# Performance work log

Hardware: AMD Instinct MI355X
Metric: run time of the kernel (lower is better)

The kernel has to match this reference:

```python
import jax, jax.numpy as jnp
import numpy as np

B, S, D = 4, 2048, 2048   # batch, seq, hidden
E, F, K = 8, 1024, 2      # experts, expert ffn dim, top-k
SF = 1024                 # shared-expert ffn dim
EPS = 1e-6


def setup_inputs() -> dict:
    key = jax.random.key(0)
    ks = jax.random.split(key, 9)
    g = lambda k, shape, scale: (jax.random.normal(k, shape, jnp.float32) * scale)
    return {
        "x": g(ks[0], (B, S, D), 1.0),
        "rms_weight": jnp.ones((D,), jnp.float32),
        "router_w": g(ks[1], (D, E), 0.02),
        "w_gate": g(ks[2], (E, D, F), 0.02),
        "w_up": g(ks[3], (E, D, F), 0.02),
        "w_down": g(ks[4], (E, F, D), 0.02),
        "sw_gate": g(ks[5], (D, SF), 0.02),
        "sw_up": g(ks[6], (D, SF), 0.02),
        "sw_down": g(ks[7], (SF, D), 0.02),
    }


def _rmsnorm(x, w, eps=EPS):
    var = jnp.mean(x * x, axis=-1, keepdims=True)
    return x * jax.lax.rsqrt(var + eps) * w


def reference(x, rms_weight, router_w, w_gate, w_up, w_down, sw_gate, sw_up, sw_down):
    b, s, d = x.shape
    e = router_w.shape[1]
    h = _rmsnorm(x, rms_weight)
    ht = h.reshape(-1, d)                      # [T, D] tokens
    t = ht.shape[0]

    # Router: softmax over experts, top-k, renormalize selected weights
    logits = ht @ router_w                     # [T, E]
    probs = jax.nn.softmax(logits, axis=-1)
    topv, topi = jax.lax.top_k(probs, K)       # [T, K]
    topv = topv / jnp.sum(topv, axis=-1, keepdims=True)
    # dense [T, E] combine weights (zero for non-selected experts)
    w_dense = jnp.zeros((t, e), ht.dtype).at[jnp.arange(t)[:, None], topi].set(topv)

    # Expert SwiGLU MLPs (grouped GEMM expressed densely over experts)
    g = jnp.einsum('td,edf->tef', ht, w_gate)  # [T, E, F]
    u = jnp.einsum('td,edf->tef', ht, w_up)
    eo = jnp.einsum('tef,efd->ted', jax.nn.silu(g) * u, w_down)  # [T, E, D]
    moe = jnp.einsum('te,ted->td', w_dense, eo)                   # weighted combine

    # Shared expert (SwiGLU)
    sh = (jax.nn.silu(ht @ sw_gate) * (ht @ sw_up)) @ sw_down

    return (moe + sh).reshape(b, s, d)
```

## Files before the change

kernel.cpp:

```cpp
#include <hip/hip_runtime.h>
#include <stdint.h>

#define T_TOK 8192
#define DDIM  2048
#define NEXP  8
#define FDIM  1024
#define CAP   25600
#define NT_M  200
#define BK    64
#define GXT   16
#define NBLK  (GXT * NT_M)
#define CPX   (NBLK / 8)

typedef __bf16 bf16x8 __attribute__((ext_vector_type(8)));
typedef float  f32x4  __attribute__((ext_vector_type(4)));

typedef const __attribute__((address_space(1))) uint32_t* as1_u32;
typedef __attribute__((address_space(3))) uint32_t* as3_u32;

__device__ __forceinline__ void gload16(const void* g, void* l) {
  __builtin_amdgcn_global_load_lds((as1_u32)g, (as3_u32)l, 16, 0, 0);
}
__device__ __forceinline__ float bf2f(uint16_t u) {
  union { uint32_t i; float f; } v; v.i = ((uint32_t)u) << 16; return v.f;
}
__device__ __forceinline__ uint16_t f2bf(float f) {
  union { float f; uint32_t i; } v; v.f = f;
  uint32_t i = v.i;
  i += 0x7FFFu + ((i >> 16) & 1u);
  return (uint16_t)(i >> 16);
}

__global__ __launch_bounds__(256) void k_rms_router(
    const float* __restrict__ x, const float* __restrict__ rmsw,
    const float* __restrict__ router_w, uint16_t* __restrict__ h,
    int* __restrict__ topi, float* __restrict__ topw, int* __restrict__ counts)
{
  int wv = threadIdx.x >> 6, lane = threadIdx.x & 63;
  int t = blockIdx.x * 4 + wv;
  const float* xr = x + (size_t)t * DDIM;

  float4 xv[8], wv8[8];
  #pragma unroll
  for (int j = 0; j < 8; j++) {
    xv[j]  = ((const float4*)xr)[j * 64 + lane];
    wv8[j] = ((const float4*)rmsw)[j * 64 + lane];
  }
  float ss = 0.f;
  #pragma unroll
  for (int j = 0; j < 8; j++)
    ss += xv[j].x * xv[j].x + xv[j].y * xv[j].y + xv[j].z * xv[j].z + xv[j].w * xv[j].w;
  #pragma unroll
  for (int m = 32; m >= 1; m >>= 1) ss += __shfl_xor(ss, m, 64);
  float scale = rsqrtf(ss * (1.0f / DDIM) + 1e-6f);

  float hv[8][4];
  #pragma unroll
  for (int j = 0; j < 8; j++) {
    hv[j][0] = xv[j].x * scale * wv8[j].x;
    hv[j][1] = xv[j].y * scale * wv8[j].y;
    hv[j][2] = xv[j].z * scale * wv8[j].z;
    hv[j][3] = xv[j].w * scale * wv8[j].w;
    ushort4 hw;
    hw.x = f2bf(hv[j][0]); hw.y = f2bf(hv[j][1]);
    hw.z = f2bf(hv[j][2]); hw.w = f2bf(hv[j][3]);
    ((ushort4*)(h + (size_t)t * DDIM))[j * 64 + lane] = hw;
  }

  float lp[8] = {0, 0, 0, 0, 0, 0, 0, 0};
  #pragma unroll
  for (int j = 0; j < 8; j++) {
    #pragma unroll
    for (int c = 0; c < 4; c++) {
      int d = (j * 64 + lane) * 4 + c;
      const float* rw = router_w + (size_t)d * NEXP;
      float4 a = ((const float4*)rw)[0];
      float4 b = ((const float4*)rw)[1];
      float hj = hv[j][c];
      lp[0] += hj * a.x; lp[1] += hj * a.y; lp[2] += hj * a.z; lp[3] += hj * a.w;
      lp[4] += hj * b.x; lp[5] += hj * b.y; lp[6] += hj * b.z; lp[7] += hj * b.w;
    }
  }
  #pragma unroll
  for (int m = 32; m >= 1; m >>= 1) {
    #pragma unroll
    for (int e = 0; e < 8; e++) lp[e] += __shfl_xor(lp[e], m, 64);
  }
  if (lane == 0) {
    int i0 = 0;
    for (int e = 1; e < 8; e++) if (lp[e] > lp[i0]) i0 = e;
    int i1 = (i0 == 0) ? 1 : 0;
    for (int e = 0; e < 8; e++) if (e != i0 && lp[e] > lp[i1]) i1 = e;
    float p0 = 1.f / (1.f + expf(lp[i1] - lp[i0]));
    topi[t * 2] = i0; topi[t * 2 + 1] = i1;
    topw[t * 2] = p0; topw[t * 2 + 1] = 1.f - p0;
    atomicAdd(&counts[i0], 1);
    atomicAdd(&counts[i1], 1);
  }
}

__global__ void k_offsets(const int* __restrict__ counts, int* __restrict__ off) {
  if (threadIdx.x == 0 && blockIdx.x == 0) {
    int o = 0;
    for (int e = 0; e < NEXP; e++) { off[e] = o; o += (counts[e] + 127) & ~127; }
    off[8] = o;
    off[9] = o + T_TOK;
  }
}

__global__ __launch_bounds__(256) void k_scatter(
    const int* __restrict__ topi, const float* __restrict__ topw,
    const int* __restrict__ off, int* __restrict__ cursor,
    int* __restrict__ tokslot, float* __restrict__ wtrow)
{
  int idx = blockIdx.x * 256 + threadIdx.x;
  if (idx < T_TOK * 2) {
    int t = idx >> 1, k = idx & 1;
    int e = topi[idx];
    int slot = atomicAdd(&cursor[e], 1);
    int row = off[e] + slot;
    tokslot[row] = t * 4 + k;
    wtrow[row] = topw[idx];
  } else {
    int t = idx - T_TOK * 2;
    int row = off[8] + t;
    tokslot[row] = t * 4 + 2;
    wtrow[row] = 1.0f;
  }
}

__global__ __launch_bounds__(256) void k_tr_df(
    const float* __restrict__ wg, const float* __restrict__ wu,
    const float* __restrict__ sg, const float* __restrict__ su,
    uint16_t* __restrict__ wgT, uint16_t* __restrict__ wuT,
    uint16_t* __restrict__ sgT, uint16_t* __restrict__ suT)
{
  __shared__ float tile[32][33];
  int z = blockIdx.z;
  const float* src; uint16_t* dst;
  if (z < 8)       { src = wg + (size_t)z * DDIM * FDIM;       dst = wgT + (size_t)z * FDIM * DDIM; }
  else if (z < 16) { src = wu + (size_t)(z - 8) * DDIM * FDIM; dst = wuT + (size_t)(z - 8) * FDIM * DDIM; }
  else if (z == 16){ src = sg; dst = sgT; }
  else             { src = su; dst = suT; }
  int c0 = blockIdx.x * 32, r0 = blockIdx.y * 32;
  int tx = threadIdx.x & 31, ty = threadIdx.x >> 5;
  #pragma unroll
  for (int i = 0; i < 4; i++)
    tile[ty + 8 * i][tx] = src[(size_t)(r0 + ty + 8 * i) * FDIM + c0 + tx];
  __syncthreads();
  #pragma unroll
  for (int i = 0; i < 4; i++)
    dst[(size_t)(c0 + ty + 8 * i) * DDIM + r0 + tx] = f2bf(tile[tx][ty + 8 * i]);
}

__global__ __launch_bounds__(256) void k_tr_fd(
    const float* __restrict__ wd, const float* __restrict__ sd,
    uint16_t* __restrict__ wdT, uint16_t* __restrict__ sdT)
{
  __shared__ float tile[32][33];
  int z = blockIdx.z;
  const float* src; uint16_t* dst;
  if (z < 8) { src = wd + (size_t)z * FDIM * DDIM; dst = wdT + (size_t)z * DDIM * FDIM; }
  else       { src = sd; dst = sdT; }
  int c0 = blockIdx.x * 32, r0 = blockIdx.y * 32;
  int tx = threadIdx.x & 31, ty = threadIdx.x >> 5;
  #pragma unroll
  for (int i = 0; i < 4; i++)
    tile[ty + 8 * i][tx] = src[(size_t)(r0 + ty + 8 * i) * DDIM + c0 + tx];
  __syncthreads();
  #pragma unroll
  for (int i = 0; i < 4; i++)
    dst[(size_t)(c0 + ty + 8 * i) * FDIM + r0 + tx] = f2bf(tile[tx][ty + 8 * i]);
}

#define BUFA(c) (ldsu + (size_t)(c) * 16384)
#define BUFB(c) (ldsu + 8192 + (size_t)(c) * 16384)

#define XCD_REMAP()                                                            \
  int flat_ = blockIdx.y * GXT + blockIdx.x;                                   \
  int nf_ = (flat_ & 7) * CPX + (flat_ >> 3);                                  \
  int bx = nf_ & (GXT - 1);                                                    \
  int by = nf_ / GXT;

#define STAGE8(T, C) do {                                                     \
  _Pragma("unroll") for (int i_ = 0; i_ < 4; i_++) {                          \
    int G_ = w * 256 + i_ * 64 + lane;                                        \
    gload16(aSrc[i_] + (size_t)(T) * BK, BUFA(C) + G_ * 8);                   \
    gload16(bSrc[i_] + (size_t)(T) * BK, BUFB(C) + G_ * 8);                   \
  } } while (0)

#define COMPUTE_TILE(curA, curB) do {                                         \
  _Pragma("unroll") for (int ks_ = 0; ks_ < 2; ks_++) {                       \
    int ce_ = ks_ * 32 + ((lane >> 4) << 3);                                  \
    bf16x8 av_[4], bv_[4];                                                    \
    _Pragma("unroll") for (int m_ = 0; m_ < 4; m_++) {                        \
      int rr_ = wr * 64 + m_ * 16 + (lane & 15);                              \
      av_[m_] = *(const bf16x8*)((curA) + rr_ * 64 + (ce_ ^ ((rr_ & 7) << 3))); \
    }                                                                         \
    _Pragma("unroll") for (int n_ = 0; n_ < 4; n_++) {                        \
      int rr_ = wc * 64 + n_ * 16 + (lane & 15);                              \
      bv_[n_] = *(const bf16x8*)((curB) + rr_ * 64 + (ce_ ^ ((rr_ & 7) << 3))); \
    }                                                                         \
    __builtin_amdgcn_s_setprio(1);                                            \
    _Pragma("unroll") for (int m_ = 0; m_ < 4; m_++)                          \
    _Pragma("unroll") for (int n_ = 0; n_ < 4; n_++)                          \
      acc[m_][n_] = __builtin_amdgcn_mfma_f32_16x16x32_bf16(av_[m_], bv_[n_], acc[m_][n_], 0, 0, 0); \
    __builtin_amdgcn_s_setprio(0);                                            \
  } } while (0)

__global__ __launch_bounds__(256, 2) void k_stage1(
    const uint16_t* __restrict__ h, const uint16_t* __restrict__ wgT,
    const uint16_t* __restrict__ wuT, const uint16_t* __restrict__ sgT,
    const uint16_t* __restrict__ suT, const int* __restrict__ off,
    const int* __restrict__ tokslot, uint16_t* __restrict__ A_int)
{
  __shared__ __align__(16) uint16_t ldsu[32768];

  XCD_REMAP();
  int row0 = by * 128;
  int end = off[9];
  if (row0 >= end) return;
  int e = 0;
  #pragma unroll 1
  for (; e < 9; e++) if (row0 >= off[e] && row0 < off[e + 1]) break;
  const uint16_t* bg = (e < NEXP) ? wgT + (size_t)e * FDIM * DDIM : sgT;
  const uint16_t* bu = (e < NEXP) ? wuT + (size_t)e * FDIM * DDIM : suT;
  int f0 = bx * 64;

  int tid = threadIdx.x, lane = tid & 63, w = tid >> 6;
  int wr = w & 1, wc = w >> 1;

  const uint16_t* aSrc[4];
  const uint16_t* bSrc[4];
  #pragma unroll
  for (int i = 0; i < 4; i++) {
    int G = w * 256 + i * 64 + lane;
    int r = G >> 3, sl = G & 7;
    int gl = sl ^ (r & 7);
    int ts = tokslot[row0 + r];
    int tok = ts < 0 ? 0 : (ts >> 2);
    aSrc[i] = h + (size_t)tok * DDIM + gl * 8;
    int b = r >> 4;
    int fc = f0 + ((b >> 1) << 4) + (r & 15);
    const uint16_t* wbase = (b & 1) ? bu : bg;
    bSrc[i] = wbase + (size_t)fc * DDIM + gl * 8;
  }

  f32x4 acc[4][4] = {};
  const int NT = DDIM / BK;

  STAGE8(0, 0);
  __syncthreads();

  #pragma unroll 1
  for (int t = 0; t < NT; ++t) {
    int cur = t & 1;
    if (t + 1 < NT) STAGE8(t + 1, cur ^ 1);
    const uint16_t* curA = BUFA(cur);
    const uint16_t* curB = BUFB(cur);
    COMPUTE_TILE(curA, curB);
    __syncthreads();
  }

  #pragma unroll
  for (int m = 0; m < 4; m++) {
    #pragma unroll
    for (int p = 0; p < 2; p++) {
      #pragma unroll
      for (int r = 0; r < 4; r++) {
        int row = row0 + wr * 64 + m * 16 + ((lane >> 4) << 2) + r;
        int col = f0 + wc * 32 + p * 16 + (lane & 15);
        float g = acc[m][2 * p][r];
        float u = acc[m][2 * p + 1][r];
        float a = (g / (1.f + expf(-g))) * u;
        A_int[(size_t)row * FDIM + col] = f2bf(a);
      }
    }
  }
}

__global__ __launch_bounds__(256, 2) void k_stage2(
    const uint16_t* __restrict__ A_int, const uint16_t* __restrict__ wdT,
    const uint16_t* __restrict__ sdT, const int* __restrict__ off,
    const int* __restrict__ tokslot, const float* __restrict__ wtrow,
    uint16_t* __restrict__ eo, float* __restrict__ out)
{
  __shared__ __align__(16) uint16_t ldsu[32768];

  XCD_REMAP();
  int row0 = by * 128;
  int end = off[9];
  if (row0 >= end) return;
  int e = 0;
  #pragma unroll 1
  for (; e < 9; e++) if (row0 >= off[e] && row0 < off[e + 1]) break;
  const uint16_t* bw = (e < NEXP) ? wdT + (size_t)e * DDIM * FDIM : sdT;
  int d0 = bx * 128;

  int tid = threadIdx.x, lane = tid & 63, w = tid >> 6;
  int wr = w & 1, wc = w >> 1;

  const uint16_t* aSrc[4];
  const uint16_t* bSrc[4];
  #pragma unroll
  for (int i = 0; i < 4; i++) {
    int G = w * 256 + i * 64 + lane;
    int r = G >> 3, sl = G & 7;
    int gl = sl ^ (r & 7);
    aSrc[i] = A_int + (size_t)(row0 + r) * FDIM + gl * 8;
    bSrc[i] = bw + (size_t)(d0 + r) * FDIM + gl * 8;
  }

  f32x4 acc[4][4] = {};
  const int NT = FDIM / BK;

  STAGE8(0, 0);
  __syncthreads();

  #pragma unroll 1
  for (int t = 0; t < NT; ++t) {
    int cur = t & 1;
    if (t + 1 < NT) STAGE8(t + 1, cur ^ 1);
    const uint16_t* curA = BUFA(cur);
    const uint16_t* curB = BUFB(cur);
    COMPUTE_TILE(curA, curB);
    __syncthreads();
  }

  #pragma unroll
  for (int m = 0; m < 4; m++) {
    #pragma unroll
    for (int r = 0; r < 4; r++) {
      int grow = row0 + wr * 64 + m * 16 + ((lane >> 4) << 2) + r;
      int ts = tokslot[grow];
      if (ts < 0) continue;
      int tok = ts >> 2, slot = ts & 3;
      if (slot == 2) {
        size_t obase = (size_t)tok * DDIM;
        #pragma unroll
        for (int n = 0; n < 4; n++) {
          int col = d0 + wc * 64 + n * 16 + (lane & 15);
          out[obase + col] = acc[m][n][r];
        }
      } else {
        float wt = wtrow[grow];
        size_t obase = ((size_t)tok * 2 + slot) * DDIM;
        #pragma unroll
        for (int n = 0; n < 4; n++) {
          int col = d0 + wc * 64 + n * 16 + (lane & 15);
          eo[obase + col] = f2bf(acc[m][n][r] * wt);
        }
      }
    }
  }
}

__global__ __launch_bounds__(256) void k_final(
    const uint16_t* __restrict__ eo, float* __restrict__ out)
{
  int tok = blockIdx.x;
  int col = threadIdx.x * 8;
  const uint16_t* e0 = eo + ((size_t)tok * 2) * DDIM + col;
  const uint16_t* e1 = eo + ((size_t)tok * 2 + 1) * DDIM + col;
  float* op = out + (size_t)tok * DDIM + col;
  ushort4 a0 = *(const ushort4*)(e0);
  ushort4 a1 = *(const ushort4*)(e0 + 4);
  ushort4 b0 = *(const ushort4*)(e1);
  ushort4 b1 = *(const ushort4*)(e1 + 4);
  float4 s0 = *(const float4*)(op);
  float4 s1 = *(const float4*)(op + 4);
  float4 o0, o1;
  o0.x = s0.x + bf2f(a0.x) + bf2f(b0.x);
  o0.y = s0.y + bf2f(a0.y) + bf2f(b0.y);
  o0.z = s0.z + bf2f(a0.z) + bf2f(b0.z);
  o0.w = s0.w + bf2f(a0.w) + bf2f(b0.w);
  o1.x = s1.x + bf2f(a1.x) + bf2f(b1.x);
  o1.y = s1.y + bf2f(a1.y) + bf2f(b1.y);
  o1.z = s1.z + bf2f(a1.z) + bf2f(b1.z);
  o1.w = s1.w + bf2f(a1.w) + bf2f(b1.w);
  *(float4*)(op) = o0;
  *(float4*)(op + 4) = o1;
}

extern "C" void kernel_launch(void* const* d_in, const int* in_sizes, int n_in,
                              void* d_out, int out_size, void* d_ws, size_t ws_size,
                              hipStream_t stream) {
  (void)in_sizes; (void)n_in; (void)out_size;
  const float* x    = (const float*)d_in[0];
  const float* rmsw = (const float*)d_in[1];
  const float* rtw  = (const float*)d_in[2];
  const float* wg   = (const float*)d_in[3];
  const float* wu   = (const float*)d_in[4];
  const float* wd   = (const float*)d_in[5];
  const float* sg   = (const float*)d_in[6];
  const float* su   = (const float*)d_in[7];
  const float* sd   = (const float*)d_in[8];
  float* out = (float*)d_out;

  char* base = (char*)d_ws;
  size_t off_b = 0;
  auto place = [&](size_t bytes) { size_t r = off_b; off_b += (bytes + 255) & ~(size_t)255; return r; };
  size_t o_topi    = place((size_t)T_TOK * 2 * 4);
  size_t o_topw    = place((size_t)T_TOK * 2 * 4);
  size_t o_counts  = place(64);
  size_t o_offs    = place(64);
  size_t o_cursor  = place(64);
  size_t o_tokslot = place((size_t)CAP * 4);
  size_t o_wtrow   = place((size_t)CAP * 4);
  size_t o_h   = place((size_t)T_TOK * DDIM * 2);
  size_t o_wgT = place((size_t)NEXP * FDIM * DDIM * 2);
  size_t o_wuT = place((size_t)NEXP * FDIM * DDIM * 2);
  size_t o_sgT = place((size_t)FDIM * DDIM * 2);
  size_t o_suT = place((size_t)FDIM * DDIM * 2);
  size_t o_wdT = place((size_t)NEXP * DDIM * FDIM * 2);
  size_t o_sdT = place((size_t)DDIM * FDIM * 2);
  size_t o_Ai  = place((size_t)CAP * FDIM * 2);
  size_t o_eo  = o_h;
  size_t NEED = off_b;
  if (ws_size < NEED) return;

  int*      topi    = (int*)(base + o_topi);
  float*    topw    = (float*)(base + o_topw);
  int*      counts  = (int*)(base + o_counts);
  int*      offs    = (int*)(base + o_offs);
  int*      cursor  = (int*)(base + o_cursor);
  int*      tokslot = (int*)(base + o_tokslot);
  float*    wtrow   = (float*)(base + o_wtrow);
  uint16_t* h       = (uint16_t*)(base + o_h);
  uint16_t* wgT     = (uint16_t*)(base + o_wgT);
  uint16_t* wuT     = (uint16_t*)(base + o_wuT);
  uint16_t* sgT     = (uint16_t*)(base + o_sgT);
  uint16_t* suT     = (uint16_t*)(base + o_suT);
  uint16_t* wdT     = (uint16_t*)(base + o_wdT);
  uint16_t* sdT     = (uint16_t*)(base + o_sdT);
  uint16_t* Ai      = (uint16_t*)(base + o_Ai);
  uint16_t* eo      = (uint16_t*)(base + o_eo);

  hipMemsetAsync(counts, 0, 64, stream);
  hipMemsetAsync(cursor, 0, 64, stream);
  hipMemsetAsync(tokslot, 0xFF, (size_t)CAP * 4, stream);

  k_tr_df<<<dim3(FDIM / 32, DDIM / 32, 18), 256, 0, stream>>>(wg, wu, sg, su, wgT, wuT, sgT, suT);
  k_tr_fd<<<dim3(DDIM / 32, FDIM / 32, 9),  256, 0, stream>>>(wd, sd, wdT, sdT);

  k_rms_router<<<T_TOK / 4, 256, 0, stream>>>(x, rmsw, rtw, h, topi, topw, counts);
  k_offsets<<<1, 64, 0, stream>>>(counts, offs);
  k_scatter<<<(T_TOK * 3) / 256, 256, 0, stream>>>(topi, topw, offs, cursor, tokslot, wtrow);

  k_stage1<<<dim3(GXT, NT_M), 256, 0, stream>>>(h, wgT, wuT, sgT, suT, offs, tokslot, Ai);
  k_stage2<<<dim3(GXT, NT_M), 256, 0, stream>>>(Ai, wdT, sdT, offs, tokslot, wtrow, eo, out);
  k_final<<<T_TOK, 256, 0, stream>>>(eo, out);
}
```

Measured before the change: 746.0 us.

## Interleave global-to-LDS staging across four compute phases with vmcnt waits

Measured after the change: 812.9 us. 9.0% more time.

```diff
diff --git a/kernel.cpp b/kernel.cpp
--- a/kernel.cpp
+++ b/kernel.cpp
@@ -182,31 +182,70 @@
   int bx = nf_ & (GXT - 1);                                                    \
   int by = nf_ / GXT;
 
-#define STAGE8(T, C) do {                                                     \
-  _Pragma("unroll") for (int i_ = 0; i_ < 4; i_++) {                          \
-    int G_ = w * 256 + i_ * 64 + lane;                                        \
-    gload16(aSrc[i_] + (size_t)(T) * BK, BUFA(C) + G_ * 8);                   \
-    gload16(bSrc[i_] + (size_t)(T) * BK, BUFB(C) + G_ * 8);                   \
-  } } while (0)
-
-#define COMPUTE_TILE(curA, curB) do {                                         \
-  _Pragma("unroll") for (int ks_ = 0; ks_ < 2; ks_++) {                       \
-    int ce_ = ks_ * 32 + ((lane >> 4) << 3);                                  \
-    bf16x8 av_[4], bv_[4];                                                    \
-    _Pragma("unroll") for (int m_ = 0; m_ < 4; m_++) {                        \
-      int rr_ = wr * 64 + m_ * 16 + (lane & 15);                              \
-      av_[m_] = *(const bf16x8*)((curA) + rr_ * 64 + (ce_ ^ ((rr_ & 7) << 3))); \
-    }                                                                         \
-    _Pragma("unroll") for (int n_ = 0; n_ < 4; n_++) {                        \
-      int rr_ = wc * 64 + n_ * 16 + (lane & 15);                              \
-      bv_[n_] = *(const bf16x8*)((curB) + rr_ * 64 + (ce_ ^ ((rr_ & 7) << 3))); \
-    }                                                                         \
-    __builtin_amdgcn_s_setprio(1);                                            \
-    _Pragma("unroll") for (int m_ = 0; m_ < 4; m_++)                          \
-    _Pragma("unroll") for (int n_ = 0; n_ < 4; n_++)                          \
-      acc[m_][n_] = __builtin_amdgcn_mfma_f32_16x16x32_bf16(av_[m_], bv_[n_], acc[m_][n_], 0, 0, 0); \
-    __builtin_amdgcn_s_setprio(0);                                            \
-  } } while (0)
+#define VMC8() asm volatile("s_waitcnt vmcnt(8)" ::: "memory")
+#define VMC0() asm volatile("s_waitcnt vmcnt(0)" ::: "memory")
+
+#define STG_A02(T, C) do { if ((w & 1) == 0) {                                 \
+  _Pragma("unroll") for (int i_ = 0; i_ < 4; i_++) {                           \
+    int G_ = w * 256 + i_ * 64 + lane;                                         \
+    gload16(aSrc[i_] + (size_t)(T) * BK, BUFA(C) + G_ * 8); } } } while (0)
+#define STG_B02(T, C) do { if ((w & 1) == 0) {                                 \
+  _Pragma("unroll") for (int i_ = 0; i_ < 4; i_++) {                           \
+    int G_ = w * 256 + i_ * 64 + lane;                                         \
+    gload16(bSrc[i_] + (size_t)(T) * BK, BUFB(C) + G_ * 8); } } } while (0)
+#define STG_A13(T, C) do { if ((w & 1) == 1) {                                 \
+  _Pragma("unroll") for (int i_ = 0; i_ < 4; i_++) {                           \
+    int G_ = w * 256 + i_ * 64 + lane;                                         \
+    gload16(aSrc[i_] + (size_t)(T) * BK, BUFA(C) + G_ * 8); } } } while (0)
+#define STG_B13(T, C) do { if ((w & 1) == 1) {                                 \
+  _Pragma("unroll") for (int i_ = 0; i_ < 4; i_++) {                           \
+    int G_ = w * 256 + i_ * 64 + lane;                                         \
+    gload16(bSrc[i_] + (size_t)(T) * BK, BUFB(C) + G_ * 8); } } } while (0)
+
+#define PH(MH, NH, WAIT_CODE, STAGE_CODE) do {                                 \
+  WAIT_CODE;                                                                   \
+  __builtin_amdgcn_s_barrier();                                                \
+  __builtin_amdgcn_sched_barrier(0);                                           \
+  STAGE_CODE;                                                                  \
+  bf16x8 av_[2][2], bv_[2][2];                                                 \
+  _Pragma("unroll") for (int mi_ = 0; mi_ < 2; mi_++) {                        \
+    int rr_ = wr * 64 + ((MH) * 2 + mi_) * 16 + (lane & 15);                   \
+    _Pragma("unroll") for (int ks_ = 0; ks_ < 2; ks_++) {                      \
+      int ce_ = ks_ * 32 + ((lane >> 4) << 3);                                 \
+      av_[mi_][ks_] = *(const bf16x8*)(curA + rr_ * 64 + (ce_ ^ ((rr_ & 7) << 3))); \
+    } }                                                                        \
+  _Pragma("unroll") for (int ni_ = 0; ni_ < 2; ni_++) {                        \
+    int rr_ = wc * 64 + ((NH) * 2 + ni_) * 16 + (lane & 15);                   \
+    _Pragma("unroll") for (int ks_ = 0; ks_ < 2; ks_++) {                      \
+      int ce_ = ks_ * 32 + ((lane >> 4) << 3);                                 \
+      bv_[ni_][ks_] = *(const bf16x8*)(curB + rr_ * 64 + (ce_ ^ ((rr_ & 7) << 3))); \
+    } }                                                                        \
+  __builtin_amdgcn_s_setprio(1);                                               \
+  _Pragma("unroll") for (int mi_ = 0; mi_ < 2; mi_++)                          \
+  _Pragma("unroll") for (int ni_ = 0; ni_ < 2; ni_++)                          \
+  _Pragma("unroll") for (int ks_ = 0; ks_ < 2; ks_++)                          \
+    acc[(MH) * 2 + mi_][(NH) * 2 + ni_] = __builtin_amdgcn_mfma_f32_16x16x32_bf16( \
+        av_[mi_][ks_], bv_[ni_][ks_], acc[(MH) * 2 + mi_][(NH) * 2 + ni_], 0, 0, 0); \
+  __builtin_amdgcn_s_setprio(0);                                               \
+} while (0)
+
+#define GEMM_LOOP(NT) do {                                                     \
+  STG_A02(0, 0); STG_B02(0, 0); STG_A13(0, 0); STG_B13(0, 0);                  \
+  STG_A02(1, 1); STG_B02(1, 1);                                                \
+  _Pragma("unroll 1")                                                          \
+  for (int t = 0; t < (NT); ++t) {                                             \
+    int cur = t & 1;                                                           \
+    const uint16_t* curA = BUFA(cur);                                          \
+    const uint16_t* curB = BUFB(cur);                                          \
+    PH(0, 0, { if (t + 2 < (NT)) { VMC8(); } else { VMC0(); } },               \
+             { if (t + 1 < (NT)) { STG_A13(t + 1, cur ^ 1); STG_B13(t + 1, cur ^ 1); } }); \
+    PH(0, 1, { VMC8(); }, {});                                                 \
+    PH(1, 0, {}, { if (t + 2 < (NT)) STG_A02(t + 2, cur); });                  \
+    PH(1, 1, {}, { if (t + 2 < (NT)) STG_B02(t + 2, cur); });                  \
+  }                                                                            \
+  VMC0();                                                                      \
+  __builtin_amdgcn_s_barrier();                                                \
+} while (0)
 
 __global__ __launch_bounds__(256, 2) void k_stage1(
     const uint16_t* __restrict__ h, const uint16_t* __restrict__ wgT,
@@ -247,20 +286,7 @@
   }
 
   f32x4 acc[4][4] = {};
-  const int NT = DDIM / BK;
-
-  STAGE8(0, 0);
-  __syncthreads();
-
-  #pragma unroll 1
-  for (int t = 0; t < NT; ++t) {
-    int cur = t & 1;
-    if (t + 1 < NT) STAGE8(t + 1, cur ^ 1);
-    const uint16_t* curA = BUFA(cur);
-    const uint16_t* curB = BUFB(cur);
-    COMPUTE_TILE(curA, curB);
-    __syncthreads();
-  }
+  GEMM_LOOP(DDIM / BK);
 
   #pragma unroll
   for (int m = 0; m < 4; m++) {
@@ -312,20 +338,7 @@
   }
 
   f32x4 acc[4][4] = {};
-  const int NT = FDIM / BK;
-
-  STAGE8(0, 0);
-  __syncthreads();
-
-  #pragma unroll 1
-  for (int t = 0; t < NT; ++t) {
-    int cur = t & 1;
-    if (t + 1 < NT) STAGE8(t + 1, cur ^ 1);
-    const uint16_t* curA = BUFA(cur);
-    const uint16_t* curB = BUFB(cur);
-    COMPUTE_TILE(curA, curB);
-    __syncthreads();
-  }
+  GEMM_LOOP(FDIM / BK);
 
   #pragma unroll
   for (int m = 0; m < 4; m++) {
```
